# Performance work log

Measured on AMD Instinct MI355X. Metric: run time of the kernel, lower is better.

## Reference

```python
import jax, jax.numpy as jnp
import numpy as np

HEADS = 4
DIM_HEAD = 32


def setup_inputs() -> dict:
    key = jax.random.key(0)
    k1, k2, k3, k4 = jax.random.split(key, 4)
    dim = 64
    hidden = HEADS * DIM_HEAD  # 128
    x = jax.random.normal(k1, (1, dim, 16, 16, 16), jnp.float32)
    # Conv3d 1x1 kernels collapse to [out_ch, in_ch] matrices
    w_qkv = jax.random.normal(k2, (hidden * 3, dim), jnp.float32) * 0.05
    w_out = jax.random.normal(k3, (dim, hidden), jnp.float32) * 0.05
    b_out = jax.random.normal(k4, (dim,), jnp.float32) * 0.05
    return {"x": x, "w_qkv": w_qkv, "w_out": w_out, "b_out": b_out}


def reference(x, w_qkv, w_out, b_out):
    scale = DIM_HEAD ** -0.5
    b, c, dz, dy, dx = x.shape
    n = dz * dy * dx
    xf = x.reshape(b, c, n)  # flatten spatial dims
    # 1x1 Conv3d (no bias) == channel matmul: [b, 3*hidden, n]
    qkv = jnp.einsum('oc,bcn->bon', w_qkv, xf)
    q, k, v = jnp.split(qkv, 3, axis=1)  # each [b, hidden, n]
    def split_heads(t):
        return t.reshape(b, HEADS, DIM_HEAD, n)  # [b, h, d, n]
    q, k, v = split_heads(q), split_heads(k), split_heads(v)
    q = q * scale
    # sim[b,h,i,j] = sum_d q[b,h,d,i] k[b,h,d,j]
    sim = jnp.einsum('bhdi,bhdj->bhij', q, k)
    sim = sim - jax.lax.stop_gradient(jnp.max(sim, axis=-1, keepdims=True))
    attn = jax.nn.softmax(sim, axis=-1)
    # out[b,h,i,d] = sum_j attn[b,h,i,j] v[b,h,d,j]
    out = jnp.einsum('bhij,bhdj->bhid', attn, v)
    # 'b h (z y x) d -> b (h d) z y x'
    out = out.transpose(0, 1, 3, 2).reshape(b, HEADS * DIM_HEAD, n)
    # final 1x1 Conv3d with bias
    y = jnp.einsum('oc,bcn->bon', w_out, out) + b_out[None, :, None]
    return y.reshape(b, -1, dz, dy, dx)
```

## Files before the change

### kernel.cpp

```cpp
#include <hip/hip_runtime.h>


typedef _Float16 f16x8 __attribute__((ext_vector_type(8)));
typedef _Float16 f16x4 __attribute__((ext_vector_type(4)));
typedef _Float16 f16x2v __attribute__((ext_vector_type(2)));
typedef float f32x4 __attribute__((ext_vector_type(4)));

static __device__ inline f16x4 pack4(float a, float b, float c, float d) {
  f16x4 r;
  r.x = (_Float16)a; r.y = (_Float16)b; r.z = (_Float16)c; r.w = (_Float16)d;
  return r;
}
static __device__ inline f16x2v pack2(float a, float b) {
  f16x2v r;
  r.x = (_Float16)a; r.y = (_Float16)b;
  return r;
}

__global__ __launch_bounds__(256) void qkv_kernel(
    const float* __restrict__ x, const float* __restrict__ w,
    _Float16* __restrict__ qo, _Float16* __restrict__ ko, _Float16* __restrict__ vo,
    float* __restrict__ zero_base)
{
  __shared__ __align__(16) float xs[64 * 68];
  __shared__ __align__(16) float wsb[32 * 68];
  const int t = threadIdx.x;
  {
    int gid = (blockIdx.y * gridDim.x + blockIdx.x) * 256 + t;
    if (gid < 135168) {
      float4 z = {0.f, 0.f, 0.f, 0.f};
      *reinterpret_cast<float4*>(&zero_base[gid * 4]) = z;
    }
  }
  const int n0 = blockIdx.x * 64;
  const int o0 = blockIdx.y * 32;
  #pragma unroll
  for (int i = 0; i < 4; ++i) {
    int ch = t + i * 256;
    int c = ch >> 4, p = ch & 15;
    *reinterpret_cast<float4*>(&xs[c * 68 + p * 4]) =
        *reinterpret_cast<const float4*>(&x[c * 4096 + n0 + p * 4]);
  }
  #pragma unroll
  for (int i = 0; i < 2; ++i) {
    int ch = t + i * 256;
    int o = ch >> 4, p = ch & 15;
    *reinterpret_cast<float4*>(&wsb[o * 68 + p * 4]) =
        *reinterpret_cast<const float4*>(&w[(o0 + o) * 64 + p * 4]);
  }
  __syncthreads();
  const int oL = (t >> 5) * 4;
  const int nL = (t & 31) * 2;
  float acc[4][2] = {};
  for (int c4 = 0; c4 < 64; c4 += 4) {
    float2 xa[4];
    #pragma unroll
    for (int k = 0; k < 4; ++k)
      xa[k] = *reinterpret_cast<const float2*>(&xs[(c4 + k) * 68 + nL]);
    #pragma unroll
    for (int i = 0; i < 4; ++i) {
      float4 wv = *reinterpret_cast<const float4*>(&wsb[(oL + i) * 68 + c4]);
      acc[i][0] += wv.x * xa[0].x + wv.y * xa[1].x + wv.z * xa[2].x + wv.w * xa[3].x;
      acc[i][1] += wv.x * xa[0].y + wv.y * xa[1].y + wv.z * xa[2].y + wv.w * xa[3].y;
    }
  }
  const float qs = 0.17677669529663689f * 1.4426950408889634f;
  if (o0 < 128) {
    int ho = o0 >> 5;
    #pragma unroll
    for (int j = 0; j < 2; ++j) {
      int n = n0 + nL + j;
      *reinterpret_cast<f16x4*>(&qo[(ho * 4096 + n) * 32 + oL]) =
          pack4(acc[0][j] * qs, acc[1][j] * qs, acc[2][j] * qs, acc[3][j] * qs);
    }
  } else if (o0 < 256) {
    int ho = (o0 - 128) >> 5;
    #pragma unroll
    for (int j = 0; j < 2; ++j) {
      int n = n0 + nL + j;
      *reinterpret_cast<f16x4*>(&ko[(ho * 4096 + n) * 32 + oL]) =
          pack4(acc[0][j], acc[1][j], acc[2][j], acc[3][j]);
    }
  } else {
    #pragma unroll
    for (int i = 0; i < 4; ++i) {
      *reinterpret_cast<f16x2v*>(&vo[(size_t)(o0 - 256 + oL + i) * 4096 + n0 + nL]) =
          pack2(acc[i][0], acc[i][1]);
    }
  }
}

__global__ __launch_bounds__(256, 4) void attn_kernel(
    const _Float16* __restrict__ qg, const _Float16* __restrict__ kg,
    const _Float16* __restrict__ vg, float* __restrict__ Oacc,
    float* __restrict__ lacc, int jlen)
{
  __shared__ __align__(16) _Float16 Ks[2][64 * 40];
  __shared__ __align__(16) _Float16 Vs[2][32 * 72];
  const int t = threadIdx.x;
  const int ck = blockIdx.x;
  const int qt = blockIdx.y;
  const int h  = blockIdx.z;
  const int w = t >> 6;
  const int lane = t & 63;
  const int m = lane & 15;
  const int quad = lane >> 4;
  const int qw = qt * 256 + w * 64;

  f16x8 aq[4];
  #pragma unroll
  for (int g = 0; g < 4; ++g)
    aq[g] = *reinterpret_cast<const f16x8*>(
        &qg[(h * 4096 + qw + g * 16 + m) * 32 + quad * 8]);

  f32x4 acc[4][2];
  #pragma unroll
  for (int g = 0; g < 4; ++g) {
    acc[g][0] = f32x4{0.f, 0.f, 0.f, 0.f};
    acc[g][1] = f32x4{0.f, 0.f, 0.f, 0.f};
  }
  float ls[4] = {0.f, 0.f, 0.f, 0.f};

  const int jbeg = ck * jlen;
  const int kr = t >> 2, ksg = t & 3;
  const int vr = t >> 3, vsg = t & 7;
  const _Float16* kgp = kg + (size_t)(h * 4096 + jbeg + kr) * 32 + ksg * 8;
  const _Float16* vgp = vg + (size_t)(h * 32 + vr) * 4096 + jbeg + vsg * 8;

  *reinterpret_cast<uint4*>(&Ks[0][kr * 40 + ksg * 8]) =
      *reinterpret_cast<const uint4*>(kgp);
  *reinterpret_cast<uint4*>(&Vs[0][vr * 72 + vsg * 8]) =
      *reinterpret_cast<const uint4*>(vgp);
  __syncthreads();

  for (int it = 0; it < jlen; it += 64) {
    const int buf = (it >> 6) & 1;
    if (it + 64 < jlen) {
      *reinterpret_cast<uint4*>(&Ks[buf ^ 1][kr * 40 + ksg * 8]) =
          *reinterpret_cast<const uint4*>(kgp + (size_t)(it + 64) * 32);
      *reinterpret_cast<uint4*>(&Vs[buf ^ 1][vr * 72 + vsg * 8]) =
          *reinterpret_cast<const uint4*>(vgp + it + 64);
    }
    #pragma unroll
    for (int jt = 0; jt < 4; ++jt) {
      f16x8 kf = *reinterpret_cast<const f16x8*>(&Ks[buf][(jt * 16 + m) * 40 + quad * 8]);
      f16x4 vf0 = *reinterpret_cast<const f16x4*>(&Vs[buf][m * 72 + jt * 16 + quad * 4]);
      f16x4 vf1 = *reinterpret_cast<const f16x4*>(&Vs[buf][(16 + m) * 72 + jt * 16 + quad * 4]);
      f32x4 z = {0.f, 0.f, 0.f, 0.f};
      f32x4 sT[4];
      #pragma unroll
      for (int g = 0; g < 4; ++g)
        sT[g] = __builtin_amdgcn_mfma_f32_16x16x32_f16(kf, aq[g], z, 0, 0, 0);
      #pragma unroll
      for (int g = 0; g < 4; ++g) {
        float p0 = exp2f(sT[g][0]), p1 = exp2f(sT[g][1]);
        float p2 = exp2f(sT[g][2]), p3 = exp2f(sT[g][3]);
        ls[g] += (p0 + p1) + (p2 + p3);
        f16x4 p = pack4(p0, p1, p2, p3);
        acc[g][0] = __builtin_amdgcn_mfma_f32_16x16x16f16(p, vf0, acc[g][0], 0, 0, 0);
        acc[g][1] = __builtin_amdgcn_mfma_f32_16x16x16f16(p, vf1, acc[g][1], 0, 0, 0);
      }
    }
    __syncthreads();
  }

  #pragma unroll
  for (int g = 0; g < 4; ++g) {
    ls[g] += __shfl_xor(ls[g], 16);
    ls[g] += __shfl_xor(ls[g], 32);
  }
  #pragma unroll
  for (int g = 0; g < 4; ++g) {
    #pragma unroll
    for (int dt = 0; dt < 2; ++dt) {
      #pragma unroll
      for (int r = 0; r < 4; ++r) {
        int q = qw + g * 16 + quad * 4 + r;
        atomicAdd(&Oacc[q * 128 + h * 32 + dt * 16 + m], acc[g][dt][r]);
      }
    }
  }
  if (quad == 0) {
    #pragma unroll
    for (int g = 0; g < 4; ++g)
      atomicAdd(&lacc[h * 4096 + qw + g * 16 + m], ls[g]);
  }
}

__global__ __launch_bounds__(256) void out_kernel(
    const float* __restrict__ Oacc, const float* __restrict__ lacc,
    const float* __restrict__ wo, const float* __restrict__ bo,
    float* __restrict__ y)
{
  __shared__ __align__(16) float as[16 * 132];
  __shared__ __align__(16) float wsh[64 * 132];
  const int t = threadIdx.x;
  const int nb = blockIdx.x * 16;
  {
    int ch = t;
    #pragma unroll
    for (int i = 0; i < 2; ++i, ch += 256) {
      int r = ch >> 5, p = ch & 31;
      float4 o4 = *reinterpret_cast<const float4*>(&Oacc[(nb + r) * 128 + p * 4]);
      float inv = 1.0f / lacc[(p >> 3) * 4096 + nb + r];
      o4.x *= inv; o4.y *= inv; o4.z *= inv; o4.w *= inv;
      *reinterpret_cast<float4*>(&as[r * 132 + p * 4]) = o4;
    }
  }
  {
    int ch = t;
    #pragma unroll
    for (int i = 0; i < 8; ++i, ch += 256) {
      int r = ch >> 5, p = ch & 31;
      *reinterpret_cast<float4*>(&wsh[r * 132 + p * 4]) =
          *reinterpret_cast<const float4*>(&wo[r * 128 + p * 4]);
    }
  }
  __syncthreads();
  const int oL = (t >> 4) * 4;
  const int n = t & 15;
  float acc[4] = {0.f, 0.f, 0.f, 0.f};
  for (int c = 0; c < 128; c += 4) {
    float4 a = *reinterpret_cast<const float4*>(&as[n * 132 + c]);
    #pragma unroll
    for (int i = 0; i < 4; ++i) {
      float4 wv = *reinterpret_cast<const float4*>(&wsh[(oL + i) * 132 + c]);
      acc[i] += wv.x * a.x + wv.y * a.y + wv.z * a.z + wv.w * a.w;
    }
  }
  #pragma unroll
  for (int i = 0; i < 4; ++i) {
    y[(size_t)(oL + i) * 4096 + nb + n] = acc[i] + bo[oL + i];
  }
}

extern "C" void kernel_launch(void* const* d_in, const int* in_sizes, int n_in,
                              void* d_out, int out_size, void* d_ws, size_t ws_size,
                              hipStream_t stream) {
  (void)in_sizes; (void)n_in; (void)out_size; (void)ws_size;
  const float* x     = (const float*)d_in[0];
  const float* w_qkv = (const float*)d_in[1];
  const float* w_out = (const float*)d_in[2];
  const float* b_out = (const float*)d_in[3];
  float* y = (float*)d_out;
  _Float16* qb = (_Float16*)d_ws;
  _Float16* kb = qb + 524288;
  _Float16* vb = kb + 524288;
  float* Oacc  = (float*)(vb + 524288);
  float* lacc  = Oacc + 524288;

  qkv_kernel<<<dim3(64, 12), 256, 0, stream>>>(x, w_qkv, qb, kb, vb, Oacc);
  attn_kernel<<<dim3(8, 16, 4), 256, 0, stream>>>(qb, kb, vb, Oacc, lacc, 4096 / 8);
  out_kernel<<<256, 256, 0, stream>>>(Oacc, lacc, w_out, b_out, y);
}
```

Before: 106.0 us.

## Replace atomic split-K reduction with per-chunk partial buffers reduced in output kernel

The attention kernel no longer atomically adds into a shared accumulator. Each key chunk now writes its own partial O and row sum to a separate buffer, and the output kernel adds the 8 chunk partials before normalising. This removes the zeroing pass in the qkv kernel and the atomic contention. Each block now covers 128 queries instead of 256, which doubles the grid size but halves Q reuse per K/V tile. The cost is 8x more partial data written and then read back from global memory.

Result: faster. 103.2 us (-2.7%).

```diff
diff --git a/kernel.cpp b/kernel.cpp
--- a/kernel.cpp
+++ b/kernel.cpp
@@ -19,19 +19,11 @@
 
 __global__ __launch_bounds__(256) void qkv_kernel(
     const float* __restrict__ x, const float* __restrict__ w,
-    _Float16* __restrict__ qo, _Float16* __restrict__ ko, _Float16* __restrict__ vo,
-    float* __restrict__ zero_base)
+    _Float16* __restrict__ qo, _Float16* __restrict__ ko, _Float16* __restrict__ vo)
 {
   __shared__ __align__(16) float xs[64 * 68];
   __shared__ __align__(16) float wsb[32 * 68];
   const int t = threadIdx.x;
-  {
-    int gid = (blockIdx.y * gridDim.x + blockIdx.x) * 256 + t;
-    if (gid < 135168) {
-      float4 z = {0.f, 0.f, 0.f, 0.f};
-      *reinterpret_cast<float4*>(&zero_base[gid * 4]) = z;
-    }
-  }
   const int n0 = blockIdx.x * 64;
   const int o0 = blockIdx.y * 32;
   #pragma unroll
@@ -92,8 +84,8 @@
 
 __global__ __launch_bounds__(256, 4) void attn_kernel(
     const _Float16* __restrict__ qg, const _Float16* __restrict__ kg,
-    const _Float16* __restrict__ vg, float* __restrict__ Oacc,
-    float* __restrict__ lacc, int jlen)
+    const _Float16* __restrict__ vg, float* __restrict__ Opart,
+    float* __restrict__ lpart, int jlen)
 {
   __shared__ __align__(16) _Float16 Ks[2][64 * 40];
   __shared__ __align__(16) _Float16 Vs[2][32 * 72];
@@ -105,21 +97,21 @@
   const int lane = t & 63;
   const int m = lane & 15;
   const int quad = lane >> 4;
-  const int qw = qt * 256 + w * 64;
-
-  f16x8 aq[4];
-  #pragma unroll
-  for (int g = 0; g < 4; ++g)
+  const int qw = qt * 128 + w * 32;
+
+  f16x8 aq[2];
+  #pragma unroll
+  for (int g = 0; g < 2; ++g)
     aq[g] = *reinterpret_cast<const f16x8*>(
         &qg[(h * 4096 + qw + g * 16 + m) * 32 + quad * 8]);
 
-  f32x4 acc[4][2];
-  #pragma unroll
-  for (int g = 0; g < 4; ++g) {
+  f32x4 acc[2][2];
+  #pragma unroll
+  for (int g = 0; g < 2; ++g) {
     acc[g][0] = f32x4{0.f, 0.f, 0.f, 0.f};
     acc[g][1] = f32x4{0.f, 0.f, 0.f, 0.f};
   }
-  float ls[4] = {0.f, 0.f, 0.f, 0.f};
+  float ls[2] = {0.f, 0.f};
 
   const int jbeg = ck * jlen;
   const int kr = t >> 2, ksg = t & 3;
@@ -147,12 +139,12 @@
       f16x4 vf0 = *reinterpret_cast<const f16x4*>(&Vs[buf][m * 72 + jt * 16 + quad * 4]);
       f16x4 vf1 = *reinterpret_cast<const f16x4*>(&Vs[buf][(16 + m) * 72 + jt * 16 + quad * 4]);
       f32x4 z = {0.f, 0.f, 0.f, 0.f};
-      f32x4 sT[4];
-      #pragma unroll
-      for (int g = 0; g < 4; ++g)
+      f32x4 sT[2];
+      #pragma unroll
+      for (int g = 0; g < 2; ++g)
         sT[g] = __builtin_amdgcn_mfma_f32_16x16x32_f16(kf, aq[g], z, 0, 0, 0);
       #pragma unroll
-      for (int g = 0; g < 4; ++g) {
+      for (int g = 0; g < 2; ++g) {
         float p0 = exp2f(sT[g][0]), p1 = exp2f(sT[g][1]);
         float p2 = exp2f(sT[g][2]), p3 = exp2f(sT[g][3]);
         ls[g] += (p0 + p1) + (p2 + p3);
@@ -165,47 +157,46 @@
   }
 
   #pragma unroll
-  for (int g = 0; g < 4; ++g) {
+  for (int g = 0; g < 2; ++g) {
     ls[g] += __shfl_xor(ls[g], 16);
     ls[g] += __shfl_xor(ls[g], 32);
   }
-  #pragma unroll
-  for (int g = 0; g < 4; ++g) {
+  const size_t cb = (size_t)(ck * 4 + h) * 4096;
+  #pragma unroll
+  for (int g = 0; g < 2; ++g) {
     #pragma unroll
     for (int dt = 0; dt < 2; ++dt) {
       #pragma unroll
       for (int r = 0; r < 4; ++r) {
         int q = qw + g * 16 + quad * 4 + r;
-        atomicAdd(&Oacc[q * 128 + h * 32 + dt * 16 + m], acc[g][dt][r]);
+        Opart[(cb + q) * 32 + dt * 16 + m] = acc[g][dt][r];
       }
     }
   }
   if (quad == 0) {
     #pragma unroll
-    for (int g = 0; g < 4; ++g)
-      atomicAdd(&lacc[h * 4096 + qw + g * 16 + m], ls[g]);
+    for (int g = 0; g < 2; ++g)
+      lpart[cb + qw + g * 16 + m] = ls[g];
   }
 }
 
 __global__ __launch_bounds__(256) void out_kernel(
-    const float* __restrict__ Oacc, const float* __restrict__ lacc,
+    const float* __restrict__ Opart, const float* __restrict__ lpart,
     const float* __restrict__ wo, const float* __restrict__ bo,
     float* __restrict__ y)
 {
   __shared__ __align__(16) float as[16 * 132];
   __shared__ __align__(16) float wsh[64 * 132];
+  __shared__ float linv[64];
   const int t = threadIdx.x;
   const int nb = blockIdx.x * 16;
-  {
-    int ch = t;
-    #pragma unroll
-    for (int i = 0; i < 2; ++i, ch += 256) {
-      int r = ch >> 5, p = ch & 31;
-      float4 o4 = *reinterpret_cast<const float4*>(&Oacc[(nb + r) * 128 + p * 4]);
-      float inv = 1.0f / lacc[(p >> 3) * 4096 + nb + r];
-      o4.x *= inv; o4.y *= inv; o4.z *= inv; o4.w *= inv;
-      *reinterpret_cast<float4*>(&as[r * 132 + p * 4]) = o4;
-    }
+  if (t < 64) {
+    int h = t >> 4, r = t & 15;
+    float s = 0.f;
+    #pragma unroll
+    for (int ck = 0; ck < 8; ++ck)
+      s += lpart[(size_t)(ck * 4 + h) * 4096 + nb + r];
+    linv[t] = 1.f / s;
   }
   {
     int ch = t;
@@ -214,6 +205,25 @@
       int r = ch >> 5, p = ch & 31;
       *reinterpret_cast<float4*>(&wsh[r * 132 + p * 4]) =
           *reinterpret_cast<const float4*>(&wo[r * 128 + p * 4]);
+    }
+  }
+  __syncthreads();
+  {
+    int ch = t;
+    #pragma unroll
+    for (int i = 0; i < 2; ++i, ch += 256) {
+      int r = ch >> 5, p = ch & 31;
+      int h = p >> 3, d4 = (p & 7) * 4;
+      float4 s = {0.f, 0.f, 0.f, 0.f};
+      #pragma unroll
+      for (int ck = 0; ck < 8; ++ck) {
+        float4 o4 = *reinterpret_cast<const float4*>(
+            &Opart[((size_t)(ck * 4 + h) * 4096 + nb + r) * 32 + d4]);
+        s.x += o4.x; s.y += o4.y; s.z += o4.z; s.w += o4.w;
+      }
+      float inv = linv[h * 16 + r];
+      s.x *= inv; s.y *= inv; s.z *= inv; s.w *= inv;
+      *reinterpret_cast<float4*>(&as[r * 132 + p * 4]) = s;
     }
   }
   __syncthreads();
@@ -246,10 +256,10 @@
   _Float16* qb = (_Float16*)d_ws;
   _Float16* kb = qb + 524288;
   _Float16* vb = kb + 524288;
-  float* Oacc  = (float*)(vb + 524288);
-  float* lacc  = Oacc + 524288;
-
-  qkv_kernel<<<dim3(64, 12), 256, 0, stream>>>(x, w_qkv, qb, kb, vb, Oacc);
-  attn_kernel<<<dim3(8, 16, 4), 256, 0, stream>>>(qb, kb, vb, Oacc, lacc, 4096 / 8);
-  out_kernel<<<256, 256, 0, stream>>>(Oacc, lacc, w_out, b_out, y);
-}
+  float* Opart = (float*)(vb + 524288);
+  float* lpart = Opart + 4194304;
+
+  qkv_kernel<<<dim3(64, 12), 256, 0, stream>>>(x, w_qkv, qb, kb, vb);
+  attn_kernel<<<dim3(8, 32, 4), 256, 0, stream>>>(qb, kb, vb, Opart, lpart, 4096 / 8);
+  out_kernel<<<256, 256, 0, stream>>>(Opart, lpart, w_out, b_out, y);
+}
```
